# Optimization experiments

Hardware: AMD Instinct MI355X
Metric: run time of the kernel (lower is better)

The kernel has to match this reference:

```python
import jax, jax.numpy as jnp
import numpy as np

JET_FEATURES_WEIGHT = 1.0


def setup_inputs() -> dict:
    key = jax.random.key(0)
    k1, k2 = jax.random.split(key)
    B, N, D = 64, 2048, 4
    p = jax.random.normal(k1, (B, N, D), dtype=jnp.float32)
    q = jax.random.normal(k2, (B, N, D), dtype=jnp.float32)
    return {"p": p, "q": q}


def reference(p, q):
    # pairwise squared Euclidean (cartesian norm) distances via the
    # |p|^2 + |q|^2 - 2 p.q expansion (avoids a (B,N,N,4) broadcast temp)
    p_sq = jnp.sum(p * p, axis=-1)                      # (B, N)
    q_sq = jnp.sum(q * q, axis=-1)                      # (B, N)
    cross = jnp.einsum("bnd,bmd->bnm", p, q)            # (B, N, N)
    dist = p_sq[:, :, None] + q_sq[:, None, :] - 2.0 * cross  # (B, N, N)

    min_pq = jnp.min(dist, axis=-1)                     # (B, N) nearest q for each p
    min_qp = jnp.min(dist, axis=-2)                     # (B, N) nearest p for each q
    chamfer_loss = jnp.sum(min_pq + min_qp)

    # jet-level term: normsq of the difference of total 4-momenta
    jet_diff = jnp.sum(p, axis=-2) - jnp.sum(q, axis=-2)  # (B, 4)
    jet_loss = jnp.sum(jet_diff * jet_diff)

    return chamfer_loss + JET_FEATURES_WEIGHT * jet_loss
```

## Files before the change

kernel.cpp:

```cpp
#include <hip/hip_runtime.h>

#define N_PTS  2048
#define BATCH  64
#define NSLICE 16
#define SLICE  (N_PTS / NSLICE)
#define P      16
#define BLK    128
#define NGROUP (2 * BATCH)
#define QBLK4  (N_PTS / 4 / 256)

static_assert(P * BLK == N_PTS, "each block covers all queries of its (b,dir)");
static_assert(SLICE == BLK, "staging assumes one point per thread");

__device__ __forceinline__ int fkey(float v) {
    int b = __float_as_int(v);
    return b >= 0 ? b : b ^ 0x7fffffff;
}
__device__ __forceinline__ float funkey(int b) {
    return __int_as_float(b >= 0 ? b : b ^ 0x7fffffff);
}

template <bool ATOMIC>
__global__ __launch_bounds__(BLK, 4) void chamfer_partial(
        const float4* __restrict__ p,
        const float4* __restrict__ q,
        float* __restrict__ wpart,
        float* __restrict__ out) {
    __shared__ float4 sQ[SLICE];
    __shared__ float4 sQs4[SLICE / 4];

    const int tid = threadIdx.x;
    const int s   = blockIdx.x;
    const int b   = blockIdx.y;
    const int dir = blockIdx.z;
    const int g   = dir * BATCH + b;
    const float4* __restrict__ A  = dir ? q : p;
    const float4* __restrict__ Bm = dir ? p : q;
    const float4* __restrict__ Ab = A  + (size_t)b * N_PTS;
    const float4* __restrict__ Bb = Bm + (size_t)b * N_PTS + s * SLICE;

    if (s == 0 && b == 0 && dir == 0 && tid == 0) out[0] = 0.0f;

    {
        const float4 v = Bb[tid];
        sQ[tid] = v;
        ((float*)sQs4)[tid] = v.x * v.x + v.y * v.y + v.z * v.z + v.w * v.w;
    }
    __syncthreads();

    float4 pm[P];
    float  mn[P];
#pragma unroll
    for (int k = 0; k < P; ++k) {
        const float4 pv = Ab[tid + k * BLK];
        pm[k] = make_float4(-2.0f * pv.x, -2.0f * pv.y, -2.0f * pv.z, -2.0f * pv.w);
        mn[k] = 3.4e38f;
    }

#pragma unroll 1
    for (int j = 0; j < SLICE; j += 4) {
        const float4 qs = sQs4[j >> 2];
        const float4 q0 = sQ[j + 0];
        const float4 q1 = sQ[j + 1];
        const float4 q2 = sQ[j + 2];
        const float4 q3 = sQ[j + 3];
#pragma unroll
        for (int k = 0; k < P; ++k) {
            float t0 = fmaf(pm[k].x, q0.x, qs.x);
            t0 = fmaf(pm[k].y, q0.y, t0);
            t0 = fmaf(pm[k].z, q0.z, t0);
            t0 = fmaf(pm[k].w, q0.w, t0);
            float t1 = fmaf(pm[k].x, q1.x, qs.y);
            t1 = fmaf(pm[k].y, q1.y, t1);
            t1 = fmaf(pm[k].z, q1.z, t1);
            t1 = fmaf(pm[k].w, q1.w, t1);
            asm("v_min3_f32 %0, %0, %1, %2" : "+v"(mn[k]) : "v"(t0), "v"(t1));
            float t2 = fmaf(pm[k].x, q2.x, qs.z);
            t2 = fmaf(pm[k].y, q2.y, t2);
            t2 = fmaf(pm[k].z, q2.z, t2);
            t2 = fmaf(pm[k].w, q2.w, t2);
            float t3 = fmaf(pm[k].x, q3.x, qs.w);
            t3 = fmaf(pm[k].y, q3.y, t3);
            t3 = fmaf(pm[k].z, q3.z, t3);
            t3 = fmaf(pm[k].w, q3.w, t3);
            asm("v_min3_f32 %0, %0, %1, %2" : "+v"(mn[k]) : "v"(t2), "v"(t3));
        }
    }

    if (ATOMIC) {
        int* wi = (int*)wpart + (size_t)g * N_PTS;
#pragma unroll
        for (int k = 0; k < P; ++k) {
            const float4 m = pm[k];
            const float psq = 0.25f * (m.x * m.x + m.y * m.y + m.z * m.z + m.w * m.w);
            atomicMin(wi + tid + k * BLK, fkey(mn[k] + psq));
        }
    } else {
        float* wf = wpart + ((size_t)g * NSLICE + s) * N_PTS;
#pragma unroll
        for (int k = 0; k < P; ++k) {
            const float4 m = pm[k];
            const float psq = 0.25f * (m.x * m.x + m.y * m.y + m.z * m.z + m.w * m.w);
            wf[tid + k * BLK] = mn[k] + psq;
        }
    }
}

template <bool ATOMIC>
__global__ __launch_bounds__(256) void chamfer_finish(
        const float4* __restrict__ p,
        const float4* __restrict__ q,
        const float* __restrict__ wpart,
        float* __restrict__ out) {
    __shared__ float wred[4];
    __shared__ float4 wacc[4];
    const int tid  = threadIdx.x;
    const int qi4  = blockIdx.x * 256 + tid;
    const int b    = blockIdx.y;
    const int dir  = blockIdx.z;
    const int g    = dir * BATCH + b;
    const int lane = tid & 63;
    const int wid  = tid >> 6;

    float acc;
    if (ATOMIC) {
        const int4 v = ((const int4*)wpart)[(size_t)g * (N_PTS / 4) + qi4];
        acc = funkey(v.x) + funkey(v.y) + funkey(v.z) + funkey(v.w);
    } else {
        const float4* wf = (const float4*)wpart + (size_t)g * NSLICE * (N_PTS / 4);
        float4 m = wf[qi4];
#pragma unroll
        for (int s2 = 1; s2 < NSLICE; ++s2) {
            const float4 v = wf[(size_t)s2 * (N_PTS / 4) + qi4];
            m.x = fminf(m.x, v.x); m.y = fminf(m.y, v.y);
            m.z = fminf(m.z, v.z); m.w = fminf(m.w, v.w);
        }
        acc = (m.x + m.y) + (m.z + m.w);
    }

#pragma unroll
    for (int off = 32; off > 0; off >>= 1) acc += __shfl_down(acc, off, 64);
    if (lane == 0) wred[wid] = acc;
    __syncthreads();
    if (tid == 0) {
        atomicAdd(out, wred[0] + wred[1] + wred[2] + wred[3]);
    }

    if (dir == 0 && blockIdx.x == 0) {
        const float4* __restrict__ Pb = p + (size_t)b * N_PTS;
        const float4* __restrict__ Qb = q + (size_t)b * N_PTS;
        float ax = 0.f, ay = 0.f, az = 0.f, aw = 0.f;
        for (int j = tid; j < N_PTS; j += 256) {
            const float4 pv = Pb[j];
            const float4 qv = Qb[j];
            ax += pv.x - qv.x;
            ay += pv.y - qv.y;
            az += pv.z - qv.z;
            aw += pv.w - qv.w;
        }
#pragma unroll
        for (int off = 32; off > 0; off >>= 1) {
            ax += __shfl_down(ax, off, 64);
            ay += __shfl_down(ay, off, 64);
            az += __shfl_down(az, off, 64);
            aw += __shfl_down(aw, off, 64);
        }
        if (lane == 0) wacc[wid] = make_float4(ax, ay, az, aw);
        __syncthreads();
        if (tid == 0) {
            float dx = 0.f, dy = 0.f, dz = 0.f, dw = 0.f;
#pragma unroll
            for (int w = 0; w < 4; ++w) {
                dx += wacc[w].x; dy += wacc[w].y; dz += wacc[w].z; dw += wacc[w].w;
            }
            atomicAdd(out, dx * dx + dy * dy + dz * dz + dw * dw);
        }
    }
}

extern "C" void kernel_launch(void* const* d_in, const int* in_sizes, int n_in,
                              void* d_out, int out_size, void* d_ws, size_t ws_size,
                              hipStream_t stream) {
    const float4* p = (const float4*)d_in[0];
    const float4* q = (const float4*)d_in[1];
    float* out = (float*)d_out;
    float* ws  = (float*)d_ws;

    const size_t part_plain  = (size_t)NGROUP * NSLICE * N_PTS * sizeof(float);
    const size_t part_atomic = (size_t)NGROUP * N_PTS * sizeof(int);

    if (ws_size >= part_plain) {
        chamfer_partial<false><<<dim3(NSLICE, BATCH, 2), BLK, 0, stream>>>(p, q, ws, out);
        chamfer_finish<false><<<dim3(QBLK4, BATCH, 2), 256, 0, stream>>>(p, q, ws, out);
    } else {
        hipMemsetAsync(ws, 0x7F, part_atomic, stream);
        chamfer_partial<true><<<dim3(NSLICE, BATCH, 2), BLK, 0, stream>>>(p, q, ws, out);
        chamfer_finish<true><<<dim3(QBLK4, BATCH, 2), 256, 0, stream>>>(p, q, ws, out);
    }
}
```

Measured before the change: 116.3 us.

## Compute distance matrix once and derive both row and column minima

Replaces the two-direction launch, which recomputed the full p-q distance matrix for the q-to-p minima, with a single pass. Each block keeps per-row minima in registers and reduces column minima across the wavefront with shuffles plus LDS atomicMin, writing them to a separate workspace. The |p|^2 term is folded into the distance accumulation, and the block shape changes to 256 threads with 8 rows each. This roughly halves the FMA work but adds per-step cross-lane shuffle reductions and shared atomics.

New measurement: 106.1 us. 8.7% less time.

```diff
diff --git a/kernel.cpp b/kernel.cpp
--- a/kernel.cpp
+++ b/kernel.cpp
@@ -4,13 +4,11 @@
 #define BATCH  64
 #define NSLICE 16
 #define SLICE  (N_PTS / NSLICE)
-#define P      16
-#define BLK    128
-#define NGROUP (2 * BATCH)
-#define QBLK4  (N_PTS / 4 / 256)
-
-static_assert(P * BLK == N_PTS, "each block covers all queries of its (b,dir)");
-static_assert(SLICE == BLK, "staging assumes one point per thread");
+#define P      8
+#define BLK    256
+
+static_assert(P * BLK == N_PTS, "block must cover all rows for col-final mins");
+static_assert(SLICE <= BLK, "one staged point per thread");
 
 __device__ __forceinline__ int fkey(float v) {
     int b = __float_as_int(v);
@@ -21,40 +19,43 @@
 }
 
 template <bool ATOMIC>
-__global__ __launch_bounds__(BLK, 4) void chamfer_partial(
+__global__ __launch_bounds__(BLK)
+__attribute__((amdgpu_waves_per_eu(4, 4)))
+void chamfer_partial(
         const float4* __restrict__ p,
         const float4* __restrict__ q,
-        float* __restrict__ wpart,
+        float* __restrict__ wrow,
+        float* __restrict__ wcol,
         float* __restrict__ out) {
     __shared__ float4 sQ[SLICE];
     __shared__ float4 sQs4[SLICE / 4];
+    __shared__ int    colk[SLICE];
 
     const int tid = threadIdx.x;
     const int s   = blockIdx.x;
     const int b   = blockIdx.y;
-    const int dir = blockIdx.z;
-    const int g   = dir * BATCH + b;
-    const float4* __restrict__ A  = dir ? q : p;
-    const float4* __restrict__ Bm = dir ? p : q;
-    const float4* __restrict__ Ab = A  + (size_t)b * N_PTS;
-    const float4* __restrict__ Bb = Bm + (size_t)b * N_PTS + s * SLICE;
-
-    if (s == 0 && b == 0 && dir == 0 && tid == 0) out[0] = 0.0f;
-
-    {
-        const float4 v = Bb[tid];
+    const float4* __restrict__ Pb = p + (size_t)b * N_PTS;
+    const float4* __restrict__ Qb = q + (size_t)b * N_PTS + s * SLICE;
+
+    if (s == 0 && b == 0 && tid == 0) out[0] = 0.0f;
+
+    if (tid < SLICE) {
+        const float4 v = Qb[tid];
         sQ[tid] = v;
         ((float*)sQs4)[tid] = v.x * v.x + v.y * v.y + v.z * v.z + v.w * v.w;
+        colk[tid] = 0x7FFFFFFF;
     }
     __syncthreads();
 
     float4 pm[P];
+    float  psq[P];
     float  mn[P];
 #pragma unroll
     for (int k = 0; k < P; ++k) {
-        const float4 pv = Ab[tid + k * BLK];
-        pm[k] = make_float4(-2.0f * pv.x, -2.0f * pv.y, -2.0f * pv.z, -2.0f * pv.w);
-        mn[k] = 3.4e38f;
+        const float4 pv = Pb[tid + k * BLK];
+        psq[k] = pv.x * pv.x + pv.y * pv.y + pv.z * pv.z + pv.w * pv.w;
+        pm[k]  = make_float4(-2.0f * pv.x, -2.0f * pv.y, -2.0f * pv.z, -2.0f * pv.w);
+        mn[k]  = 3.4e38f;
     }
 
 #pragma unroll 1
@@ -64,70 +65,91 @@
         const float4 q1 = sQ[j + 1];
         const float4 q2 = sQ[j + 2];
         const float4 q3 = sQ[j + 3];
-#pragma unroll
-        for (int k = 0; k < P; ++k) {
-            float t0 = fmaf(pm[k].x, q0.x, qs.x);
-            t0 = fmaf(pm[k].y, q0.y, t0);
-            t0 = fmaf(pm[k].z, q0.z, t0);
-            t0 = fmaf(pm[k].w, q0.w, t0);
-            float t1 = fmaf(pm[k].x, q1.x, qs.y);
-            t1 = fmaf(pm[k].y, q1.y, t1);
-            t1 = fmaf(pm[k].z, q1.z, t1);
-            t1 = fmaf(pm[k].w, q1.w, t1);
-            asm("v_min3_f32 %0, %0, %1, %2" : "+v"(mn[k]) : "v"(t0), "v"(t1));
-            float t2 = fmaf(pm[k].x, q2.x, qs.z);
-            t2 = fmaf(pm[k].y, q2.y, t2);
-            t2 = fmaf(pm[k].z, q2.z, t2);
-            t2 = fmaf(pm[k].w, q2.w, t2);
-            float t3 = fmaf(pm[k].x, q3.x, qs.w);
-            t3 = fmaf(pm[k].y, q3.y, t3);
-            t3 = fmaf(pm[k].z, q3.z, t3);
-            t3 = fmaf(pm[k].w, q3.w, t3);
-            asm("v_min3_f32 %0, %0, %1, %2" : "+v"(mn[k]) : "v"(t2), "v"(t3));
-        }
+        float c0 = 3.4e38f, c1 = 3.4e38f, c2 = 3.4e38f, c3 = 3.4e38f;
+#pragma unroll
+        for (int k = 0; k < P; k += 2) {
+            const float4 a0 = pm[k], a1 = pm[k + 1];
+            const float  e0 = psq[k], e1 = psq[k + 1];
+            float u00 = fmaf(a0.x, q0.x, qs.x + e0);
+            u00 = fmaf(a0.y, q0.y, u00); u00 = fmaf(a0.z, q0.z, u00); u00 = fmaf(a0.w, q0.w, u00);
+            float u01 = fmaf(a0.x, q1.x, qs.y + e0);
+            u01 = fmaf(a0.y, q1.y, u01); u01 = fmaf(a0.z, q1.z, u01); u01 = fmaf(a0.w, q1.w, u01);
+            float u02 = fmaf(a0.x, q2.x, qs.z + e0);
+            u02 = fmaf(a0.y, q2.y, u02); u02 = fmaf(a0.z, q2.z, u02); u02 = fmaf(a0.w, q2.w, u02);
+            float u03 = fmaf(a0.x, q3.x, qs.w + e0);
+            u03 = fmaf(a0.y, q3.y, u03); u03 = fmaf(a0.z, q3.z, u03); u03 = fmaf(a0.w, q3.w, u03);
+            float u10 = fmaf(a1.x, q0.x, qs.x + e1);
+            u10 = fmaf(a1.y, q0.y, u10); u10 = fmaf(a1.z, q0.z, u10); u10 = fmaf(a1.w, q0.w, u10);
+            float u11 = fmaf(a1.x, q1.x, qs.y + e1);
+            u11 = fmaf(a1.y, q1.y, u11); u11 = fmaf(a1.z, q1.z, u11); u11 = fmaf(a1.w, q1.w, u11);
+            float u12 = fmaf(a1.x, q2.x, qs.z + e1);
+            u12 = fmaf(a1.y, q2.y, u12); u12 = fmaf(a1.z, q2.z, u12); u12 = fmaf(a1.w, q2.w, u12);
+            float u13 = fmaf(a1.x, q3.x, qs.w + e1);
+            u13 = fmaf(a1.y, q3.y, u13); u13 = fmaf(a1.z, q3.z, u13); u13 = fmaf(a1.w, q3.w, u13);
+            asm("v_min3_f32 %0, %0, %1, %2" : "+v"(mn[k])     : "v"(u00), "v"(u01));
+            asm("v_min3_f32 %0, %0, %1, %2" : "+v"(mn[k])     : "v"(u02), "v"(u03));
+            asm("v_min3_f32 %0, %0, %1, %2" : "+v"(mn[k + 1]) : "v"(u10), "v"(u11));
+            asm("v_min3_f32 %0, %0, %1, %2" : "+v"(mn[k + 1]) : "v"(u12), "v"(u13));
+            asm("v_min3_f32 %0, %0, %1, %2" : "+v"(c0) : "v"(u00), "v"(u10));
+            asm("v_min3_f32 %0, %0, %1, %2" : "+v"(c1) : "v"(u01), "v"(u11));
+            asm("v_min3_f32 %0, %0, %1, %2" : "+v"(c2) : "v"(u02), "v"(u12));
+            asm("v_min3_f32 %0, %0, %1, %2" : "+v"(c3) : "v"(u03), "v"(u13));
+        }
+        const int l = tid & 63;
+        const float sa = (l & 1) ? c0 : c1;
+        const float sb = (l & 1) ? c2 : c3;
+        const float ka = (l & 1) ? c1 : c0;
+        const float kb = (l & 1) ? c3 : c2;
+        const float r0 = fminf(ka, __shfl_xor(sa, 1, 64));
+        const float r1 = fminf(kb, __shfl_xor(sb, 1, 64));
+        const float sc = (l & 2) ? r0 : r1;
+        const float kc = (l & 2) ? r1 : r0;
+        float m = fminf(kc, __shfl_xor(sc, 2, 64));
+        m = fminf(m, __shfl_xor(m, 4, 64));
+        m = fminf(m, __shfl_xor(m, 8, 64));
+        m = fminf(m, __shfl_xor(m, 16, 64));
+        m = fminf(m, __shfl_xor(m, 32, 64));
+        if (l < 4) atomicMin(&colk[j + l], fkey(m));
     }
 
     if (ATOMIC) {
-        int* wi = (int*)wpart + (size_t)g * N_PTS;
-#pragma unroll
-        for (int k = 0; k < P; ++k) {
-            const float4 m = pm[k];
-            const float psq = 0.25f * (m.x * m.x + m.y * m.y + m.z * m.z + m.w * m.w);
-            atomicMin(wi + tid + k * BLK, fkey(mn[k] + psq));
-        }
+        int* wi = (int*)wrow + (size_t)b * N_PTS;
+#pragma unroll
+        for (int k = 0; k < P; ++k)
+            atomicMin(wi + tid + k * BLK, fkey(mn[k]));
     } else {
-        float* wf = wpart + ((size_t)g * NSLICE + s) * N_PTS;
-#pragma unroll
-        for (int k = 0; k < P; ++k) {
-            const float4 m = pm[k];
-            const float psq = 0.25f * (m.x * m.x + m.y * m.y + m.z * m.z + m.w * m.w);
-            wf[tid + k * BLK] = mn[k] + psq;
-        }
-    }
+        float* wf = wrow + ((size_t)b * NSLICE + s) * N_PTS;
+#pragma unroll
+        for (int k = 0; k < P; ++k)
+            wf[tid + k * BLK] = mn[k];
+    }
+
+    __syncthreads();
+    if (tid < SLICE)
+        wcol[(size_t)b * N_PTS + s * SLICE + tid] = funkey(colk[tid]);
 }
 
 template <bool ATOMIC>
 __global__ __launch_bounds__(256) void chamfer_finish(
         const float4* __restrict__ p,
         const float4* __restrict__ q,
-        const float* __restrict__ wpart,
+        const float* __restrict__ wrow,
+        const float* __restrict__ wcol,
         float* __restrict__ out) {
     __shared__ float wred[4];
     __shared__ float4 wacc[4];
     const int tid  = threadIdx.x;
     const int qi4  = blockIdx.x * 256 + tid;
     const int b    = blockIdx.y;
-    const int dir  = blockIdx.z;
-    const int g    = dir * BATCH + b;
     const int lane = tid & 63;
     const int wid  = tid >> 6;
 
     float acc;
     if (ATOMIC) {
-        const int4 v = ((const int4*)wpart)[(size_t)g * (N_PTS / 4) + qi4];
+        const int4 v = ((const int4*)wrow)[(size_t)b * (N_PTS / 4) + qi4];
         acc = funkey(v.x) + funkey(v.y) + funkey(v.z) + funkey(v.w);
     } else {
-        const float4* wf = (const float4*)wpart + (size_t)g * NSLICE * (N_PTS / 4);
+        const float4* wf = (const float4*)wrow + (size_t)b * NSLICE * (N_PTS / 4);
         float4 m = wf[qi4];
 #pragma unroll
         for (int s2 = 1; s2 < NSLICE; ++s2) {
@@ -136,6 +158,10 @@
             m.z = fminf(m.z, v.z); m.w = fminf(m.w, v.w);
         }
         acc = (m.x + m.y) + (m.z + m.w);
+    }
+    {
+        const float4 cv = ((const float4*)wcol)[(size_t)b * (N_PTS / 4) + qi4];
+        acc += (cv.x + cv.y) + (cv.z + cv.w);
     }
 
 #pragma unroll
@@ -146,7 +172,7 @@
         atomicAdd(out, wred[0] + wred[1] + wred[2] + wred[3]);
     }
 
-    if (dir == 0 && blockIdx.x == 0) {
+    if (blockIdx.x == 0) {
         const float4* __restrict__ Pb = p + (size_t)b * N_PTS;
         const float4* __restrict__ Qb = q + (size_t)b * N_PTS;
         float ax = 0.f, ay = 0.f, az = 0.f, aw = 0.f;
@@ -186,15 +212,20 @@
     float* out = (float*)d_out;
     float* ws  = (float*)d_ws;
 
-    const size_t part_plain  = (size_t)NGROUP * NSLICE * N_PTS * sizeof(float);
-    const size_t part_atomic = (size_t)NGROUP * N_PTS * sizeof(int);
-
-    if (ws_size >= part_plain) {
-        chamfer_partial<false><<<dim3(NSLICE, BATCH, 2), BLK, 0, stream>>>(p, q, ws, out);
-        chamfer_finish<false><<<dim3(QBLK4, BATCH, 2), 256, 0, stream>>>(p, q, ws, out);
+    const size_t row_plain  = (size_t)BATCH * NSLICE * N_PTS;
+    const size_t row_atomic = (size_t)BATCH * N_PTS;
+    const size_t col_elems  = (size_t)BATCH * N_PTS;
+
+    if (ws_size >= (row_plain + col_elems) * sizeof(float)) {
+        float* wrow = ws;
+        float* wcol = ws + row_plain;
+        chamfer_partial<false><<<dim3(NSLICE, BATCH), BLK, 0, stream>>>(p, q, wrow, wcol, out);
+        chamfer_finish<false><<<dim3(2, BATCH), 256, 0, stream>>>(p, q, wrow, wcol, out);
     } else {
-        hipMemsetAsync(ws, 0x7F, part_atomic, stream);
-        chamfer_partial<true><<<dim3(NSLICE, BATCH, 2), BLK, 0, stream>>>(p, q, ws, out);
-        chamfer_finish<true><<<dim3(QBLK4, BATCH, 2), 256, 0, stream>>>(p, q, ws, out);
-    }
-}
+        float* wrow = ws;
+        float* wcol = ws + row_atomic;
+        hipMemsetAsync(wrow, 0x7F, row_atomic * sizeof(int), stream);
+        chamfer_partial<true><<<dim3(NSLICE, BATCH), BLK, 0, stream>>>(p, q, wrow, wcol, out);
+        chamfer_finish<true><<<dim3(2, BATCH), 256, 0, stream>>>(p, q, wrow, wcol, out);
+    }
+}
```
